# Performance work log

Measured on AMD Instinct MI355X. Metric: run time of the kernel, lower is better.

## Reference

```python
import jax, jax.numpy as jnp
import numpy as np

B, CIN, L = 4, 128, 2048
D_MODEL, D_STATE, EXPAND, HEADDIM, NGROUPS = 256, 16, 3, 3, 1
D_INNER = EXPAND * D_MODEL            # 768
NHEADS = D_INNER // HEADDIM           # 256
CONV_DIM = D_INNER + 2 * NGROUPS * D_STATE   # 800
D_IN_PROJ = 2 * D_INNER + 2 * NGROUPS * D_STATE + NHEADS  # 1824
K_PROJ, D_CONV = 4, 4
EPS = 1e-5


def setup_inputs() -> dict:
    key = jax.random.key(0)
    ks = jax.random.split(key, 9)
    x = jax.random.normal(ks[0], (B, CIN, L), jnp.float32)
    proj_w = jax.random.normal(ks[1], (D_MODEL, CIN, K_PROJ), jnp.float32) / np.float32(np.sqrt(CIN * K_PROJ))
    in_proj_w = jax.random.normal(ks[2], (D_IN_PROJ, D_MODEL), jnp.float32) / np.float32(np.sqrt(D_MODEL))
    conv_w = jax.random.normal(ks[3], (CONV_DIM, 1, D_CONV), jnp.float32) / np.float32(np.sqrt(D_CONV))
    conv_b = jax.random.normal(ks[4], (CONV_DIM,), jnp.float32) * 0.01
    # dt_bias = inverse-softplus of dt ~ LogUniform[1e-3, 1e-1] (mamba2 init)
    u = jax.random.uniform(ks[5], (NHEADS,), jnp.float32)
    dt = jnp.exp(u * np.float32(np.log(0.1) - np.log(1e-3)) + np.float32(np.log(1e-3)))
    dt_bias = dt + jnp.log(-jnp.expm1(-dt))
    A_log = jnp.log(1.0 + 15.0 * jax.random.uniform(ks[6], (NHEADS,), jnp.float32))  # A in [-16,-1]
    D_skip = jnp.ones((NHEADS,), jnp.float32)
    norm_w = jnp.ones((D_INNER,), jnp.float32)
    out_proj_w = jax.random.normal(ks[7], (D_MODEL, D_INNER), jnp.float32) / np.float32(np.sqrt(D_INNER))
    return {"x": x, "proj_w": proj_w, "in_proj_w": in_proj_w, "conv_w": conv_w,
            "conv_b": conv_b, "dt_bias": dt_bias, "A_log": A_log, "D_skip": D_skip,
            "norm_w": norm_w, "out_proj_w": out_proj_w}


def _forward(x, proj_w, in_proj_w, conv_w, conv_b, dt_bias, A_log, D_skip, norm_w, out_proj_w):
    # outer Conv1d, padding='same' (k=4 -> left 1, right 2), no bias: (B,CIN,L)->(B,D_MODEL,L)
    h = jax.lax.conv_general_dilated(x, proj_w, (1,), [(1, 2)],
                                     dimension_numbers=("NCH", "OIH", "NCH"))
    u = h.transpose(0, 2, 1)                          # (B, L, d_model)
    zxbcdt = jnp.einsum("bld,ed->ble", u, in_proj_w)  # (B, L, 1824)
    z = zxbcdt[..., :D_INNER]                                     # (B,L,768)
    xBC = zxbcdt[..., D_INNER:D_INNER + CONV_DIM]                 # (B,L,800)
    dt = zxbcdt[..., D_INNER + CONV_DIM:]                         # (B,L,256)
    dt = jax.nn.softplus(dt + dt_bias)
    # depthwise causal conv (pad d_conv-1 on left) + SiLU
    xBC_c = jax.lax.conv_general_dilated(xBC.transpose(0, 2, 1), conv_w, (1,), [(D_CONV - 1, 0)],
                                         feature_group_count=CONV_DIM,
                                         dimension_numbers=("NCH", "OIH", "NCH"))
    xBC = jax.nn.silu(xBC_c + conv_b[None, :, None]).transpose(0, 2, 1)  # (B,L,800)
    xs = xBC[..., :D_INNER].reshape(B, L, NHEADS, HEADDIM)        # (B,L,H,P)
    Bm = xBC[..., D_INNER:D_INNER + D_STATE]                      # (B,L,N) (ngroups=1)
    Cm = xBC[..., D_INNER + D_STATE:]                             # (B,L,N)
    A = -jnp.exp(A_log)                                           # (H,)

    def step(hst, inp):
        dt_t, x_t, B_t, C_t = inp                 # (B,H),(B,H,P),(B,N),(B,N)
        dA = jnp.exp(dt_t * A)[:, :, None, None]  # (B,H,1,1)
        hst = dA * hst + jnp.einsum("bh,bhp,bn->bhpn", dt_t, x_t, B_t)
        y_t = jnp.einsum("bhpn,bn->bhp", hst, C_t)
        return hst, y_t

    h0 = jnp.zeros((B, NHEADS, HEADDIM, D_STATE), x.dtype)
    _, ys = jax.lax.scan(step, h0, (dt.transpose(1, 0, 2), xs.transpose(1, 0, 2, 3),
                                    Bm.transpose(1, 0, 2), Cm.transpose(1, 0, 2)))
    y = ys.transpose(1, 0, 2, 3) + D_skip[None, None, :, None] * xs   # (B,L,H,P)
    y = y.reshape(B, L, D_INNER)
    # gated RMSNorm: gate first, then normalize (norm_before_gate=False)
    y = y * jax.nn.silu(z)
    y = y * jax.lax.rsqrt(jnp.mean(y * y, axis=-1, keepdims=True) + EPS) * norm_w
    out = jnp.einsum("ble,de->bld", y, out_proj_w)   # (B,L,d_model)
    return out.transpose(0, 2, 1)                    # (B,d_model,L)


def reference(x, proj_w, in_proj_w, conv_w, conv_b, dt_bias, A_log, D_skip, norm_w, out_proj_w):
    return _forward(x, proj_w, in_proj_w, conv_w, conv_b, dt_bias, A_log, D_skip, norm_w, out_proj_w)
```

## Files before the change

kernel.cpp:

```cpp
#include <hip/hip_runtime.h>
#include <hip/hip_fp16.h>
#include <math.h>

#define B_     4
#define CIN    128
#define LEN    2048
#define DMODEL 256
#define DSTATE 16
#define NHEADS 256
#define DINNER 768
#define CONVDIM 800
#define DINPROJ 1824
#define EPS_   1e-5f
#define CHUNK  64
#define NCHUNK 32

typedef _Float16 f16x8 __attribute__((ext_vector_type(8)));
typedef float    f32x4 __attribute__((ext_vector_type(4)));

__device__ __forceinline__ float silu_(float x){ return x / (1.0f + __expf(-x)); }
__device__ __forceinline__ float softplus_(float x){
    return x > 0.f ? x + log1pf(__expf(-x)) : log1pf(__expf(x));
}

__device__ __forceinline__ void gl2lds16(const _Float16* g, _Float16* l){
    __builtin_amdgcn_global_load_lds(
        (const __attribute__((address_space(1))) void*)g,
        (__attribute__((address_space(3))) void*)l, 16, 0, 0);
}

__global__ __launch_bounds__(256) void k_f2h3(const float* __restrict__ a0,
                                              const float* __restrict__ a1,
                                              const float* __restrict__ a2,
                                              _Float16* __restrict__ o0,
                                              _Float16* __restrict__ o1,
                                              _Float16* __restrict__ o2,
                                              int n0, int n1, int n2){
    int total = n0 + n1 + n2;
    for (int i = blockIdx.x * 256 + threadIdx.x; i < total; i += gridDim.x * 256){
        if (i < n0)            o0[i] = (_Float16)a0[i];
        else if (i < n0 + n1)  o1[i - n0] = (_Float16)a1[i - n0];
        else                   o2[i - n0 - n1] = (_Float16)a2[i - n0 - n1];
    }
}

__global__ __launch_bounds__(256) void k_im2col(const float* __restrict__ x,
                                                _Float16* __restrict__ xcol){
    __shared__ float xs[CIN][68];
    int blk = blockIdx.x;
    int b  = blk >> 5;
    int l0 = (blk & 31) << 6;
    const float* xb = x + (size_t)b * CIN * LEN;
    for (int idx = threadIdx.x; idx < CIN * 67; idx += 256){
        int ci = idx / 67, j = idx % 67;
        int gl = l0 - 1 + j;
        xs[ci][j] = (gl >= 0 && gl < LEN) ? xb[ci * LEN + gl] : 0.f;
    }
    __syncthreads();
    #pragma unroll
    for (int v = 0; v < 16; v++){
        int id = v * 256 + threadIdx.x;
        int rl = id >> 6, c = id & 63;
        f16x8 pk;
        #pragma unroll
        for (int e = 0; e < 8; e++){
            int ci = c * 2 + (e >> 2), k = e & 3;
            pk[e] = (_Float16)xs[ci][rl + k];
        }
        *(f16x8*)&xcol[((size_t)(b * LEN + l0 + rl)) * 512 + c * 8] = pk;
    }
}

template<int K, int EPI>
__global__ __launch_bounds__(256) void k_gemm(const _Float16* __restrict__ A,
                                              const _Float16* __restrict__ Bw,
                                              const float* __restrict__ dt_bias,
                                              _Float16* __restrict__ o_u,
                                              _Float16* __restrict__ o_z,
                                              _Float16* __restrict__ o_xbc,
                                              _Float16* __restrict__ o_dt,
                                              float* __restrict__ o_f){
    __shared__ __align__(16) _Float16 As[128 * 32];
    __shared__ __align__(16) _Float16 Bs[128 * 32];
    int tid  = threadIdx.x;
    int wv   = tid >> 6;
    int lane = tid & 63;
    int quad = lane >> 4;
    int l16  = lane & 15;
    int m0 = blockIdx.x * 128;
    int n0 = blockIdx.y * 128;
    int wm = (wv >> 1) * 64;
    int wn = (wv & 1) * 64;
    int srow = lane >> 2;
    int scol = (lane & 3) * 8;

    f32x4 acc[4][4];
    #pragma unroll
    for (int i = 0; i < 4; i++)
        #pragma unroll
        for (int j = 0; j < 4; j++)
            acc[i][j] = (f32x4){0.f, 0.f, 0.f, 0.f};

    for (int k0 = 0; k0 < K; k0 += 32){
        #pragma unroll
        for (int j = 0; j < 2; j++){
            int ar = m0 + wv * 32 + j * 16 + srow;
            gl2lds16(A + (size_t)ar * K + k0 + scol,
                     &As[(wv * 32 + j * 16) * 32]);
            int nr = n0 + wv * 32 + j * 16 + srow;
            if (EPI == 1) nr = nr > (DINPROJ - 1) ? (DINPROJ - 1) : nr;
            gl2lds16(Bw + (size_t)nr * K + k0 + scol,
                     &Bs[(wv * 32 + j * 16) * 32]);
        }
        __syncthreads();
        f16x8 af[4], bf[4];
        #pragma unroll
        for (int i = 0; i < 4; i++)
            af[i] = *(const f16x8*)&As[(wm + i * 16 + l16) * 32 + quad * 8];
        #pragma unroll
        for (int j = 0; j < 4; j++)
            bf[j] = *(const f16x8*)&Bs[(wn + j * 16 + l16) * 32 + quad * 8];
        #pragma unroll
        for (int i = 0; i < 4; i++)
            #pragma unroll
            for (int j = 0; j < 4; j++)
                acc[i][j] = __builtin_amdgcn_mfma_f32_16x16x32_f16(
                                af[i], bf[j], acc[i][j], 0, 0, 0);
        __syncthreads();
    }

    if (EPI == 0){
        #pragma unroll
        for (int j = 0; j < 4; j++){
            int col = n0 + wn + j * 16 + l16;
            #pragma unroll
            for (int i = 0; i < 4; i++){
                int row = m0 + wm + i * 16 + quad * 4;
                #pragma unroll
                for (int r = 0; r < 4; r++)
                    o_u[(size_t)(row + r) * DMODEL + col] = (_Float16)acc[i][j][r];
            }
        }
    } else if (EPI == 1){
        #pragma unroll
        for (int j = 0; j < 4; j++){
            int col = n0 + wn + j * 16 + l16;
            if (col < DINNER){
                #pragma unroll
                for (int i = 0; i < 4; i++){
                    int row = m0 + wm + i * 16 + quad * 4;
                    #pragma unroll
                    for (int r = 0; r < 4; r++)
                        o_z[(size_t)(row + r) * DINNER + col] = (_Float16)acc[i][j][r];
                }
            } else if (col < DINNER + CONVDIM){
                int cc = col - DINNER;
                #pragma unroll
                for (int i = 0; i < 4; i++){
                    int row = m0 + wm + i * 16 + quad * 4;
                    #pragma unroll
                    for (int r = 0; r < 4; r++)
                        o_xbc[(size_t)(row + r) * CONVDIM + cc] = (_Float16)acc[i][j][r];
                }
            } else if (col < DINPROJ){
                int hh = col - (DINNER + CONVDIM);
                float bias = dt_bias[hh];
                #pragma unroll
                for (int i = 0; i < 4; i++){
                    int row = m0 + wm + i * 16 + quad * 4;
                    #pragma unroll
                    for (int r = 0; r < 4; r++)
                        o_dt[(size_t)(row + r) * NHEADS + hh] =
                            (_Float16)softplus_(acc[i][j][r] + bias);
                }
            }
        }
    } else {
        #pragma unroll
        for (int i = 0; i < 4; i++){
            int row = m0 + wm + i * 16 + quad * 4;
            int b = row >> 11, l = row & (LEN - 1);
            #pragma unroll
            for (int j = 0; j < 4; j++){
                int d = n0 + wn + j * 16 + l16;
                *(f32x4*)&o_f[(((size_t)(b * DMODEL + d)) << 11) + l] = acc[i][j];
            }
        }
    }
}

__global__ __launch_bounds__(256) void k_dwconv(const __half* __restrict__ xbc,
                                                const float* __restrict__ cw,
                                                const float* __restrict__ cb,
                                                __half* __restrict__ xcc){
    int idx = blockIdx.x * 256 + threadIdx.x;
    int c = idx % CONVDIM;
    int r = idx / CONVDIM;
    int l = r & (LEN - 1);
    float4 wv = *(const float4*)(cw + c * 4);
    float acc = cb[c];
    if (l >= 3){
        const __half* base = xbc + (size_t)(r - 3) * CONVDIM + c;
        acc += __half2float(base[0]) * wv.x + __half2float(base[CONVDIM]) * wv.y +
               __half2float(base[2 * CONVDIM]) * wv.z + __half2float(base[3 * CONVDIM]) * wv.w;
    } else {
        const float wk[4] = {wv.x, wv.y, wv.z, wv.w};
        for (int k = 0; k < 4; k++){
            int t = l - 3 + k;
            if (t >= 0) acc += __half2float(xbc[(size_t)(r + k - 3) * CONVDIM + c]) * wk[k];
        }
    }
    xcc[idx] = __float2half(silu_(acc));
}

__global__ __launch_bounds__(64) void k_scanAC(const __half* __restrict__ dtb,
                                               const __half* __restrict__ xcc,
                                               const float* __restrict__ A_log,
                                               const float* __restrict__ D_skip,
                                               __half* __restrict__ y,
                                               __half* __restrict__ cstate,
                                               float* __restrict__ dsum){
    int blk = blockIdx.x;
    int c  = blk & (NCHUNK - 1);
    int hg = (blk >> 5) & 63;
    int b  = blk >> 11;
    int lane = threadIdx.x;
    int hl = lane >> 4;
    int n  = lane & 15;
    int h  = hg * 4 + hl;
    int c0 = h * 3;
    float A   = -__expf(A_log[h]);
    float Dsk = D_skip[h];
    int t0 = c * CHUNK;
    const __half* xr  = xcc + ((size_t)b * LEN + t0) * CONVDIM;
    const __half* dtp = dtb + ((size_t)b * LEN + t0) * NHEADS + h;
    float h0 = 0.f, h1 = 0.f, h2 = 0.f, sdt = 0.f;
    __half* yp = y + ((size_t)b * LEN + t0) * DINNER + c0;
    for (int t = 0; t < CHUNK; t++){
        float vx0 = __half2float(xr[c0]);
        float vx1 = __half2float(xr[c0 + 1]);
        float vx2 = __half2float(xr[c0 + 2]);
        float vB  = __half2float(xr[DINNER + n]);
        float vC  = __half2float(xr[DINNER + DSTATE + n]);
        float cdt = __half2float(dtp[(size_t)t * NHEADS]);
        float dA  = __expf(cdt * A);
        float dtB = cdt * vB;
        h0 = fmaf(h0, dA, vx0 * dtB);
        h1 = fmaf(h1, dA, vx1 * dtB);
        h2 = fmaf(h2, dA, vx2 * dtB);
        sdt += cdt;
        float p0 = h0 * vC, p1 = h1 * vC, p2 = h2 * vC;
        #pragma unroll
        for (int m = 1; m < 16; m <<= 1){
            p0 += __shfl_xor(p0, m, 64);
            p1 += __shfl_xor(p1, m, 64);
            p2 += __shfl_xor(p2, m, 64);
        }
        if (n < 3){
            float pv = (n == 0) ? p0 : ((n == 1) ? p1 : p2);
            float xv = (n == 0) ? vx0 : ((n == 1) ? vx1 : vx2);
            yp[n] = __float2half(fmaf(Dsk, xv, pv));
        }
        xr += CONVDIM;
        yp += DINNER;
    }
    size_t sbase = (((size_t)(b * NHEADS + h)) * NCHUNK + c) * 48;
    cstate[sbase + n]      = __float2half(h0);
    cstate[sbase + 16 + n] = __float2half(h1);
    cstate[sbase + 32 + n] = __float2half(h2);
    if (n == 0) dsum[(size_t)(b * NHEADS + h) * NCHUNK + c] = __expf(A * sdt);
}

__global__ __launch_bounds__(64) void k_scanB(__half* __restrict__ cstate,
                                              const float* __restrict__ dsum){
    int bh = blockIdx.x;
    int lane = threadIdx.x;
    if (lane >= 48) return;
    __half* st = cstate + (size_t)bh * NCHUNK * 48 + lane;
    const float* dd = dsum + (size_t)bh * NCHUNK;
    float H = 0.f;
    for (int c = 0; c < NCHUNK; c++){
        float d = dd[c];
        float s = __half2float(st[(size_t)c * 48]);
        st[(size_t)c * 48] = __float2half(H);
        H = fmaf(H, d, s);
    }
}

__global__ __launch_bounds__(256) void k_fixup(const __half* __restrict__ dtb,
                                               const __half* __restrict__ xcc,
                                               const float* __restrict__ A_log,
                                               const __half* __restrict__ cstate,
                                               __half* __restrict__ y){
    int task = blockIdx.x * 4 + (threadIdx.x >> 6);
    int lane = threadIdx.x & 63;
    int c = task & (NCHUNK - 1);
    int h = (task >> 5) & (NHEADS - 1);
    int b = task >> 13;
    float A = -__expf(A_log[h]);
    size_t row = (size_t)b * LEN + c * CHUNK + lane;
    float cum = __half2float(dtb[row * NHEADS + h]);
    #pragma unroll
    for (int m = 1; m < 64; m <<= 1){
        float v = __shfl(cum, lane - m, 64);
        if (lane >= m) cum += v;
    }
    float decay = __expf(A * cum);
    const _Float16* cp = (const _Float16*)(xcc) + row * CONVDIM + DINNER + DSTATE;
    f16x8 cv0 = *(const f16x8*)cp;
    f16x8 cv1 = *(const f16x8*)(cp + 8);
    const _Float16* hp = (const _Float16*)(cstate) + (size_t)task * 48;
    f16x8 hv[6];
    #pragma unroll
    for (int i = 0; i < 6; i++) hv[i] = *(const f16x8*)(hp + i * 8);
    float s0 = 0.f, s1 = 0.f, s2 = 0.f;
    #pragma unroll
    for (int e = 0; e < 8; e++){
        float cl = (float)cv0[e], ch = (float)cv1[e];
        s0 = fmaf(cl, (float)hv[0][e], s0); s0 = fmaf(ch, (float)hv[1][e], s0);
        s1 = fmaf(cl, (float)hv[2][e], s1); s1 = fmaf(ch, (float)hv[3][e], s1);
        s2 = fmaf(cl, (float)hv[4][e], s2); s2 = fmaf(ch, (float)hv[5][e], s2);
    }
    __half* yp = y + row * DINNER + h * 3;
    yp[0] = __float2half(__half2float(yp[0]) + decay * s0);
    yp[1] = __float2half(__half2float(yp[1]) + decay * s1);
    yp[2] = __float2half(__half2float(yp[2]) + decay * s2);
}

__global__ __launch_bounds__(256) void k_norm(__half* __restrict__ y,
                                              const __half* __restrict__ z,
                                              const float* __restrict__ nw){
    __shared__ float wsum[4];
    size_t r = blockIdx.x;
    int tid = threadIdx.x;
    const __half* zr = z + r * DINNER;
    __half* yr = y + r * DINNER;
    int e0 = tid, e1 = tid + 256, e2 = tid + 512;
    float t0 = __half2float(yr[e0]) * silu_(__half2float(zr[e0]));
    float t1 = __half2float(yr[e1]) * silu_(__half2float(zr[e1]));
    float t2 = __half2float(yr[e2]) * silu_(__half2float(zr[e2]));
    float ss = t0 * t0 + t1 * t1 + t2 * t2;
    #pragma unroll
    for (int m = 1; m < 64; m <<= 1) ss += __shfl_xor(ss, m, 64);
    if ((tid & 63) == 0) wsum[tid >> 6] = ss;
    __syncthreads();
    float tot = wsum[0] + wsum[1] + wsum[2] + wsum[3];
    float sc = rsqrtf(tot / (float)DINNER + EPS_);
    yr[e0] = __float2half(t0 * sc * nw[e0]);
    yr[e1] = __float2half(t1 * sc * nw[e1]);
    yr[e2] = __float2half(t2 * sc * nw[e2]);
}

extern "C" void kernel_launch(void* const* d_in, const int* in_sizes, int n_in,
                              void* d_out, int out_size, void* d_ws, size_t ws_size,
                              hipStream_t stream) {
    const float* x          = (const float*)d_in[0];
    const float* proj_w     = (const float*)d_in[1];
    const float* in_proj_w  = (const float*)d_in[2];
    const float* conv_w     = (const float*)d_in[3];
    const float* conv_b     = (const float*)d_in[4];
    const float* dt_bias    = (const float*)d_in[5];
    const float* A_log      = (const float*)d_in[6];
    const float* D_skip     = (const float*)d_in[7];
    const float* norm_w     = (const float*)d_in[8];
    const float* out_proj_w = (const float*)d_in[9];
    float* out = (float*)d_out;

    char* ob = (char*)d_out;
    _Float16* pw_h  = (_Float16*)ob;
    _Float16* ipw_h = (_Float16*)(ob + 262144);

    char* wsb = (char*)d_ws;
    _Float16* xcol  = (_Float16*)(wsb);
    _Float16* u_h   = (_Float16*)(wsb + 8388608);
    __half*   xcc_h = (__half*)(wsb);
    __half*   z_h   = (__half*)(wsb + 13107200);
    __half*   xbc_h = (__half*)(wsb + 25690112);
    __half*   y_h   = xbc_h;
    __half*   dt_h  = (__half*)(wsb + 38797312);
    __half*   cstate= (__half*)(wsb + 42991616);
    float*    dsum  = (float*)(wsb + 46137344);
    _Float16* opw_h = (_Float16*)(wsb + 46268416);

    k_f2h3  <<<96, 256, 0, stream>>>(proj_w, in_proj_w, out_proj_w,
                                     pw_h, ipw_h, opw_h,
                                     DMODEL * CIN * 4, DINPROJ * DMODEL,
                                     DMODEL * DINNER);
    k_im2col<<<128, 256, 0, stream>>>(x, xcol);
    k_gemm<512, 0><<<dim3(64, 2), 256, 0, stream>>>(xcol, pw_h, nullptr,
        u_h, nullptr, nullptr, nullptr, nullptr);
    k_gemm<256, 1><<<dim3(64, 15), 256, 0, stream>>>(u_h, ipw_h, dt_bias,
        nullptr, (_Float16*)z_h, (_Float16*)xbc_h, (_Float16*)dt_h, nullptr);
    k_dwconv<<<25600, 256, 0, stream>>>(xbc_h, conv_w, conv_b, xcc_h);
    k_scanAC<<<8192, 64, 0, stream>>>(dt_h, xcc_h, A_log, D_skip, y_h, cstate, dsum);
    k_scanB <<<1024, 64, 0, stream>>>(cstate, dsum);
    k_fixup <<<8192, 256, 0, stream>>>(dt_h, xcc_h, A_log, cstate, y_h);
    k_norm  <<<8192, 256, 0, stream>>>(y_h, z_h, norm_w);
    k_gemm<768, 2><<<dim3(64, 2), 256, 0, stream>>>((const _Float16*)y_h, opw_h,
        nullptr, nullptr, nullptr, nullptr, nullptr, out);
}
```

Before: 338.0 us.

## Stage scan inputs in LDS, use DPP row reductions, restructure fixup per chunk

The chunk scan now uses 256-thread blocks covering 16 heads. Each block stages the chunk's x, B/C and dt rows into shared memory with vector loads and prefetches the next timestep's values, replacing strided scalar global loads. The 16-lane shuffle reductions are replaced with DPP row-shift adds. The fixup kernel is reorganised so each block handles one half-chunk for all 256 heads: decay values are computed once into LDS and C is staged, which removes the per-task prefix-shuffle and redundant loads but cuts the grid to 256 blocks, so parallelism is much lower.

```diff
diff --git a/kernel.cpp b/kernel.cpp
--- a/kernel.cpp
+++ b/kernel.cpp
@@ -27,6 +27,15 @@
     __builtin_amdgcn_global_load_lds(
         (const __attribute__((address_space(1))) void*)g,
         (__attribute__((address_space(3))) void*)l, 16, 0, 0);
+}
+
+__device__ __forceinline__ float dpp_row_sum16(float x){
+    float v = x;
+    v += __int_as_float(__builtin_amdgcn_update_dpp(0, __float_as_int(v), 0x111, 0xf, 0xf, true));
+    v += __int_as_float(__builtin_amdgcn_update_dpp(0, __float_as_int(v), 0x112, 0xf, 0xf, true));
+    v += __int_as_float(__builtin_amdgcn_update_dpp(0, __float_as_int(v), 0x114, 0xf, 0xf, true));
+    v += __int_as_float(__builtin_amdgcn_update_dpp(0, __float_as_int(v), 0x118, 0xf, 0xf, true));
+    return v;
 }
 
 __global__ __launch_bounds__(256) void k_f2h3(const float* __restrict__ a0,
@@ -213,56 +222,87 @@
     xcc[idx] = __float2half(silu_(acc));
 }
 
-__global__ __launch_bounds__(64) void k_scanAC(const __half* __restrict__ dtb,
-                                               const __half* __restrict__ xcc,
-                                               const float* __restrict__ A_log,
-                                               const float* __restrict__ D_skip,
-                                               __half* __restrict__ y,
-                                               __half* __restrict__ cstate,
-                                               float* __restrict__ dsum){
+__global__ __launch_bounds__(256) void k_scanAC(const __half* __restrict__ dtb,
+                                                const __half* __restrict__ xcc,
+                                                const float* __restrict__ A_log,
+                                                const float* __restrict__ D_skip,
+                                                __half* __restrict__ y,
+                                                __half* __restrict__ cstate,
+                                                float* __restrict__ dsum){
+    __shared__ __align__(16) _Float16 xs_x[64][48];
+    __shared__ __align__(16) _Float16 xs_bc[64][32];
+    __shared__ __align__(16) _Float16 xs_dt[64][16];
     int blk = blockIdx.x;
-    int c  = blk & (NCHUNK - 1);
-    int hg = (blk >> 5) & 63;
-    int b  = blk >> 11;
-    int lane = threadIdx.x;
-    int hl = lane >> 4;
-    int n  = lane & 15;
-    int h  = hg * 4 + hl;
-    int c0 = h * 3;
+    int hg = blk & 15;
+    int c  = (blk >> 4) & 31;
+    int b  = blk >> 9;
+    int tid = threadIdx.x;
+    size_t row0 = (size_t)b * LEN + c * CHUNK;
+
+    const _Float16* xc16 = (const _Float16*)xcc;
+    const _Float16* dt16 = (const _Float16*)dtb;
+    #pragma unroll
+    for (int k = 0; k < 3; k++){
+        int seg = tid + k * 256;
+        if (seg < 384){
+            int t = seg / 6, k16 = seg % 6;
+            *(f16x8*)&xs_x[t][k16 * 8] =
+                *(const f16x8*)(xc16 + (row0 + t) * CONVDIM + hg * 48 + k16 * 8);
+        } else if (seg < 640){
+            int i = seg - 384; int t = i >> 2, k4 = i & 3;
+            *(f16x8*)&xs_bc[t][k4 * 8] =
+                *(const f16x8*)(xc16 + (row0 + t) * CONVDIM + DINNER + k4 * 8);
+        } else {
+            int i = seg - 640; int t = i >> 1, k2 = i & 1;
+            *(f16x8*)&xs_dt[t][k2 * 8] =
+                *(const f16x8*)(dt16 + (row0 + t) * NHEADS + hg * 16 + k2 * 8);
+        }
+    }
+    __syncthreads();
+
+    int w    = tid >> 6;
+    int lane = tid & 63;
+    int hl   = lane >> 4;
+    int n    = lane & 15;
+    int jj   = w * 4 + hl;
+    int h    = hg * 16 + jj;
+    int c0   = h * 3;
     float A   = -__expf(A_log[h]);
     float Dsk = D_skip[h];
-    int t0 = c * CHUNK;
-    const __half* xr  = xcc + ((size_t)b * LEN + t0) * CONVDIM;
-    const __half* dtp = dtb + ((size_t)b * LEN + t0) * NHEADS + h;
+
     float h0 = 0.f, h1 = 0.f, h2 = 0.f, sdt = 0.f;
-    __half* yp = y + ((size_t)b * LEN + t0) * DINNER + c0;
+    __half* yp = y + row0 * DINNER + c0;
+    float vx0 = (float)xs_x[0][jj * 3 + 0];
+    float vx1 = (float)xs_x[0][jj * 3 + 1];
+    float vx2 = (float)xs_x[0][jj * 3 + 2];
+    float vB  = (float)xs_bc[0][n];
+    float vC  = (float)xs_bc[0][16 + n];
+    float cdt = (float)xs_dt[0][jj];
     for (int t = 0; t < CHUNK; t++){
-        float vx0 = __half2float(xr[c0]);
-        float vx1 = __half2float(xr[c0 + 1]);
-        float vx2 = __half2float(xr[c0 + 2]);
-        float vB  = __half2float(xr[DINNER + n]);
-        float vC  = __half2float(xr[DINNER + DSTATE + n]);
-        float cdt = __half2float(dtp[(size_t)t * NHEADS]);
+        int tn = (t + 1 < CHUNK) ? t + 1 : t;
+        float nx0 = (float)xs_x[tn][jj * 3 + 0];
+        float nx1 = (float)xs_x[tn][jj * 3 + 1];
+        float nx2 = (float)xs_x[tn][jj * 3 + 2];
+        float nB  = (float)xs_bc[tn][n];
+        float nC  = (float)xs_bc[tn][16 + n];
+        float ndt = (float)xs_dt[tn][jj];
+
         float dA  = __expf(cdt * A);
         float dtB = cdt * vB;
         h0 = fmaf(h0, dA, vx0 * dtB);
         h1 = fmaf(h1, dA, vx1 * dtB);
         h2 = fmaf(h2, dA, vx2 * dtB);
         sdt += cdt;
-        float p0 = h0 * vC, p1 = h1 * vC, p2 = h2 * vC;
-        #pragma unroll
-        for (int m = 1; m < 16; m <<= 1){
-            p0 += __shfl_xor(p0, m, 64);
-            p1 += __shfl_xor(p1, m, 64);
-            p2 += __shfl_xor(p2, m, 64);
-        }
-        if (n < 3){
-            float pv = (n == 0) ? p0 : ((n == 1) ? p1 : p2);
-            float xv = (n == 0) ? vx0 : ((n == 1) ? vx1 : vx2);
-            yp[n] = __float2half(fmaf(Dsk, xv, pv));
-        }
-        xr += CONVDIM;
+        float p0 = dpp_row_sum16(h0 * vC);
+        float p1 = dpp_row_sum16(h1 * vC);
+        float p2 = dpp_row_sum16(h2 * vC);
+        if (n == 15){
+            yp[0] = __float2half(fmaf(Dsk, vx0, p0));
+            yp[1] = __float2half(fmaf(Dsk, vx1, p1));
+            yp[2] = __float2half(fmaf(Dsk, vx2, p2));
+        }
         yp += DINNER;
+        vx0 = nx0; vx1 = nx1; vx2 = nx2; vB = nB; vC = nC; cdt = ndt;
     }
     size_t sbase = (((size_t)(b * NHEADS + h)) * NCHUNK + c) * 48;
     cstate[sbase + n]      = __float2half(h0);
@@ -292,39 +332,60 @@
                                                const float* __restrict__ A_log,
                                                const __half* __restrict__ cstate,
                                                __half* __restrict__ y){
-    int task = blockIdx.x * 4 + (threadIdx.x >> 6);
-    int lane = threadIdx.x & 63;
-    int c = task & (NCHUNK - 1);
-    int h = (task >> 5) & (NHEADS - 1);
-    int b = task >> 13;
-    float A = -__expf(A_log[h]);
-    size_t row = (size_t)b * LEN + c * CHUNK + lane;
-    float cum = __half2float(dtb[row * NHEADS + h]);
+    __shared__ __align__(16) _Float16 decay[32][256];
+    __shared__ __align__(16) _Float16 Cs[32][16];
+    int blk = blockIdx.x;
+    int th = blk & 1;
+    int c  = (blk >> 1) & 31;
+    int b  = blk >> 6;
+    int tid = threadIdx.x;
+    int base_t = th * 32;
+    size_t row0 = (size_t)b * LEN + c * CHUNK;
+
+    if (tid < 64){
+        int i = tid >> 1, k = tid & 1;
+        *(f16x8*)&Cs[i][k * 8] =
+            *(const f16x8*)((const _Float16*)xcc +
+                            (row0 + base_t + i) * CONVDIM + DINNER + DSTATE + k * 8);
+    }
+    {
+        float A = -__expf(A_log[tid]);
+        float cum = 0.f;
+        const _Float16* dp = (const _Float16*)dtb + row0 * NHEADS + tid;
+        for (int t = 0; t < CHUNK; t++){
+            cum += (float)dp[(size_t)t * NHEADS];
+            if (t >= base_t && t < base_t + 32)
+                decay[t - base_t][tid] = (_Float16)__expf(A * cum);
+        }
+    }
+    __syncthreads();
+
+    const _Float16* hp = (const _Float16*)cstate +
+                         (((size_t)(b * NHEADS + tid)) * NCHUNK + c) * 48;
+    float Hi[3][16];
     #pragma unroll
-    for (int m = 1; m < 64; m <<= 1){
-        float v = __shfl(cum, lane - m, 64);
-        if (lane >= m) cum += v;
-    }
-    float decay = __expf(A * cum);
-    const _Float16* cp = (const _Float16*)(xcc) + row * CONVDIM + DINNER + DSTATE;
-    f16x8 cv0 = *(const f16x8*)cp;
-    f16x8 cv1 = *(const f16x8*)(cp + 8);
-    const _Float16* hp = (const _Float16*)(cstate) + (size_t)task * 48;
-    f16x8 hv[6];
-    #pragma unroll
-    for (int i = 0; i < 6; i++) hv[i] = *(const f16x8*)(hp + i * 8);
-    float s0 = 0.f, s1 = 0.f, s2 = 0.f;
-    #pragma unroll
-    for (int e = 0; e < 8; e++){
-        float cl = (float)cv0[e], ch = (float)cv1[e];
-        s0 = fmaf(cl, (float)hv[0][e], s0); s0 = fmaf(ch, (float)hv[1][e], s0);
-        s1 = fmaf(cl, (float)hv[2][e], s1); s1 = fmaf(ch, (float)hv[3][e], s1);
-        s2 = fmaf(cl, (float)hv[4][e], s2); s2 = fmaf(ch, (float)hv[5][e], s2);
-    }
-    __half* yp = y + row * DINNER + h * 3;
-    yp[0] = __float2half(__half2float(yp[0]) + decay * s0);
-    yp[1] = __float2half(__half2float(yp[1]) + decay * s1);
-    yp[2] = __float2half(__half2float(yp[2]) + decay * s2);
+    for (int p = 0; p < 3; p++){
+        f16x8 a = *(const f16x8*)(hp + p * 16);
+        f16x8 bq = *(const f16x8*)(hp + p * 16 + 8);
+        #pragma unroll
+        for (int e = 0; e < 8; e++){ Hi[p][e] = (float)a[e]; Hi[p][8 + e] = (float)bq[e]; }
+    }
+    __half* yb = y + (row0 + base_t) * DINNER + tid * 3;
+    for (int i = 0; i < 32; i++){
+        float s0 = 0.f, s1 = 0.f, s2 = 0.f;
+        #pragma unroll
+        for (int nn = 0; nn < 16; nn++){
+            float cv = (float)Cs[i][nn];
+            s0 = fmaf(cv, Hi[0][nn], s0);
+            s1 = fmaf(cv, Hi[1][nn], s1);
+            s2 = fmaf(cv, Hi[2][nn], s2);
+        }
+        float d = (float)decay[i][tid];
+        __half* yp = yb + (size_t)i * DINNER;
+        yp[0] = __float2half(__half2float(yp[0]) + d * s0);
+        yp[1] = __float2half(__half2float(yp[1]) + d * s1);
+        yp[2] = __float2half(__half2float(yp[2]) + d * s2);
+    }
 }
 
 __global__ __launch_bounds__(256) void k_norm(__half* __restrict__ y,
@@ -392,9 +453,9 @@
     k_gemm<256, 1><<<dim3(64, 15), 256, 0, stream>>>(u_h, ipw_h, dt_bias,
         nullptr, (_Float16*)z_h, (_Float16*)xbc_h, (_Float16*)dt_h, nullptr);
     k_dwconv<<<25600, 256, 0, stream>>>(xbc_h, conv_w, conv_b, xcc_h);
-    k_scanAC<<<8192, 64, 0, stream>>>(dt_h, xcc_h, A_log, D_skip, y_h, cstate, dsum);
+    k_scanAC<<<2048, 256, 0, stream>>>(dt_h, xcc_h, A_log, D_skip, y_h, cstate, dsum);
     k_scanB <<<1024, 64, 0, stream>>>(cstate, dsum);
-    k_fixup <<<8192, 256, 0, stream>>>(dt_h, xcc_h, A_log, cstate, y_h);
+    k_fixup <<<256, 256, 0, stream>>>(dt_h, xcc_h, A_log, cstate, y_h);
     k_norm  <<<8192, 256, 0, stream>>>(y_h, z_h, norm_w);
     k_gemm<768, 2><<<dim3(64, 2), 256, 0, stream>>>((const _Float16*)y_h, opw_h,
         nullptr, nullptr, nullptr, nullptr, nullptr, out);
```

Result: slower. 367.2 us (+8.6%).

## Vectorize depthwise conv, pack scan waves into blocks, restructure fixup per chunk

Applied to the files above, without the earlier changes.

The depthwise conv now has each thread handle 8 channels with 16-byte half vector loads and stores, replacing scalar per-channel accesses. The chunk scan packs four wave tasks into each 256-thread block instead of launching one 64-thread block per task. The fixup kernel is reorganised so each block covers one (batch, chunk, half-chunk) and each thread one head. Per-step decays and C vectors are staged in shared memory and the carried state is kept in registers, replacing a per-lane shuffle prefix sum and repeated state loads. The trade-off is that only 256 fixup blocks are launched, each running a serial 64-step cumulative sum, and the per-head y updates write 6-byte strided pieces.

```diff
diff --git a/kernel.cpp b/kernel.cpp
--- a/kernel.cpp
+++ b/kernel.cpp
@@ -194,37 +194,41 @@
                                                 const float* __restrict__ cb,
                                                 __half* __restrict__ xcc){
     int idx = blockIdx.x * 256 + threadIdx.x;
-    int c = idx % CONVDIM;
-    int r = idx / CONVDIM;
-    int l = r & (LEN - 1);
-    float4 wv = *(const float4*)(cw + c * 4);
-    float acc = cb[c];
-    if (l >= 3){
-        const __half* base = xbc + (size_t)(r - 3) * CONVDIM + c;
-        acc += __half2float(base[0]) * wv.x + __half2float(base[CONVDIM]) * wv.y +
-               __half2float(base[2 * CONVDIM]) * wv.z + __half2float(base[3 * CONVDIM]) * wv.w;
-    } else {
-        const float wk[4] = {wv.x, wv.y, wv.z, wv.w};
-        for (int k = 0; k < 4; k++){
-            int t = l - 3 + k;
-            if (t >= 0) acc += __half2float(xbc[(size_t)(r + k - 3) * CONVDIM + c]) * wk[k];
-        }
-    }
-    xcc[idx] = __float2half(silu_(acc));
-}
-
-__global__ __launch_bounds__(64) void k_scanAC(const __half* __restrict__ dtb,
-                                               const __half* __restrict__ xcc,
-                                               const float* __restrict__ A_log,
-                                               const float* __restrict__ D_skip,
-                                               __half* __restrict__ y,
-                                               __half* __restrict__ cstate,
-                                               float* __restrict__ dsum){
-    int blk = blockIdx.x;
-    int c  = blk & (NCHUNK - 1);
-    int hg = (blk >> 5) & 63;
-    int b  = blk >> 11;
-    int lane = threadIdx.x;
+    int seg = idx % 100;
+    int r   = idx / 100;
+    int l   = r & (LEN - 1);
+    int c8  = seg * 8;
+    const _Float16* base = (const _Float16*)xbc + (size_t)r * CONVDIM + c8;
+    f16x8 zv = {0, 0, 0, 0, 0, 0, 0, 0};
+    f16x8 x3 = *(const f16x8*)base;
+    f16x8 x2 = (l >= 1) ? *(const f16x8*)(base - CONVDIM) : zv;
+    f16x8 x1 = (l >= 2) ? *(const f16x8*)(base - 2 * CONVDIM) : zv;
+    f16x8 x0 = (l >= 3) ? *(const f16x8*)(base - 3 * CONVDIM) : zv;
+    f16x8 o;
+    #pragma unroll
+    for (int e = 0; e < 8; e++){
+        float4 wv = *(const float4*)(cw + (size_t)(c8 + e) * 4);
+        float acc = cb[c8 + e]
+                  + (float)x0[e] * wv.x + (float)x1[e] * wv.y
+                  + (float)x2[e] * wv.z + (float)x3[e] * wv.w;
+        o[e] = (_Float16)silu_(acc);
+    }
+    *(f16x8*)((_Float16*)xcc + (size_t)r * CONVDIM + c8) = o;
+}
+
+__global__ __launch_bounds__(256) void k_scanAC(const __half* __restrict__ dtb,
+                                                const __half* __restrict__ xcc,
+                                                const float* __restrict__ A_log,
+                                                const float* __restrict__ D_skip,
+                                                __half* __restrict__ y,
+                                                __half* __restrict__ cstate,
+                                                float* __restrict__ dsum){
+    int wave = threadIdx.x >> 6;
+    int task = blockIdx.x * 4 + wave;
+    int c  = task & (NCHUNK - 1);
+    int hg = (task >> 5) & 63;
+    int b  = task >> 11;
+    int lane = threadIdx.x & 63;
     int hl = lane >> 4;
     int n  = lane & 15;
     int h  = hg * 4 + hl;
@@ -292,39 +296,60 @@
                                                const float* __restrict__ A_log,
                                                const __half* __restrict__ cstate,
                                                __half* __restrict__ y){
-    int task = blockIdx.x * 4 + (threadIdx.x >> 6);
-    int lane = threadIdx.x & 63;
-    int c = task & (NCHUNK - 1);
-    int h = (task >> 5) & (NHEADS - 1);
-    int b = task >> 13;
-    float A = -__expf(A_log[h]);
-    size_t row = (size_t)b * LEN + c * CHUNK + lane;
-    float cum = __half2float(dtb[row * NHEADS + h]);
+    __shared__ __align__(16) _Float16 decay[32][256];
+    __shared__ __align__(16) _Float16 Cs[32][16];
+    int blk = blockIdx.x;
+    int th = blk & 1;
+    int c  = (blk >> 1) & 31;
+    int b  = blk >> 6;
+    int tid = threadIdx.x;
+    int base_t = th * 32;
+    size_t row0 = (size_t)b * LEN + c * CHUNK;
+
+    if (tid < 64){
+        int i = tid >> 1, k = tid & 1;
+        *(f16x8*)&Cs[i][k * 8] =
+            *(const f16x8*)((const _Float16*)xcc +
+                            (row0 + base_t + i) * CONVDIM + DINNER + DSTATE + k * 8);
+    }
+    {
+        float A = -__expf(A_log[tid]);
+        float cum = 0.f;
+        const _Float16* dp = (const _Float16*)dtb + row0 * NHEADS + tid;
+        for (int t = 0; t < CHUNK; t++){
+            cum += (float)dp[(size_t)t * NHEADS];
+            if (t >= base_t && t < base_t + 32)
+                decay[t - base_t][tid] = (_Float16)__expf(A * cum);
+        }
+    }
+    __syncthreads();
+
+    const _Float16* hp = (const _Float16*)cstate +
+                         (((size_t)(b * NHEADS + tid)) * NCHUNK + c) * 48;
+    float Hi[3][16];
     #pragma unroll
-    for (int m = 1; m < 64; m <<= 1){
-        float v = __shfl(cum, lane - m, 64);
-        if (lane >= m) cum += v;
-    }
-    float decay = __expf(A * cum);
-    const _Float16* cp = (const _Float16*)(xcc) + row * CONVDIM + DINNER + DSTATE;
-    f16x8 cv0 = *(const f16x8*)cp;
-    f16x8 cv1 = *(const f16x8*)(cp + 8);
-    const _Float16* hp = (const _Float16*)(cstate) + (size_t)task * 48;
-    f16x8 hv[6];
-    #pragma unroll
-    for (int i = 0; i < 6; i++) hv[i] = *(const f16x8*)(hp + i * 8);
-    float s0 = 0.f, s1 = 0.f, s2 = 0.f;
-    #pragma unroll
-    for (int e = 0; e < 8; e++){
-        float cl = (float)cv0[e], ch = (float)cv1[e];
-        s0 = fmaf(cl, (float)hv[0][e], s0); s0 = fmaf(ch, (float)hv[1][e], s0);
-        s1 = fmaf(cl, (float)hv[2][e], s1); s1 = fmaf(ch, (float)hv[3][e], s1);
-        s2 = fmaf(cl, (float)hv[4][e], s2); s2 = fmaf(ch, (float)hv[5][e], s2);
-    }
-    __half* yp = y + row * DINNER + h * 3;
-    yp[0] = __float2half(__half2float(yp[0]) + decay * s0);
-    yp[1] = __float2half(__half2float(yp[1]) + decay * s1);
-    yp[2] = __float2half(__half2float(yp[2]) + decay * s2);
+    for (int p = 0; p < 3; p++){
+        f16x8 a = *(const f16x8*)(hp + p * 16);
+        f16x8 bq = *(const f16x8*)(hp + p * 16 + 8);
+        #pragma unroll
+        for (int e = 0; e < 8; e++){ Hi[p][e] = (float)a[e]; Hi[p][8 + e] = (float)bq[e]; }
+    }
+    __half* yb = y + (row0 + base_t) * DINNER + tid * 3;
+    for (int i = 0; i < 32; i++){
+        float s0 = 0.f, s1 = 0.f, s2 = 0.f;
+        #pragma unroll
+        for (int nn = 0; nn < 16; nn++){
+            float cv = (float)Cs[i][nn];
+            s0 = fmaf(cv, Hi[0][nn], s0);
+            s1 = fmaf(cv, Hi[1][nn], s1);
+            s2 = fmaf(cv, Hi[2][nn], s2);
+        }
+        float d = (float)decay[i][tid];
+        __half* yp = yb + (size_t)i * DINNER;
+        yp[0] = __float2half(__half2float(yp[0]) + d * s0);
+        yp[1] = __float2half(__half2float(yp[1]) + d * s1);
+        yp[2] = __float2half(__half2float(yp[2]) + d * s2);
+    }
 }
 
 __global__ __launch_bounds__(256) void k_norm(__half* __restrict__ y,
@@ -391,10 +416,10 @@
         u_h, nullptr, nullptr, nullptr, nullptr);
     k_gemm<256, 1><<<dim3(64, 15), 256, 0, stream>>>(u_h, ipw_h, dt_bias,
         nullptr, (_Float16*)z_h, (_Float16*)xbc_h, (_Float16*)dt_h, nullptr);
-    k_dwconv<<<25600, 256, 0, stream>>>(xbc_h, conv_w, conv_b, xcc_h);
-    k_scanAC<<<8192, 64, 0, stream>>>(dt_h, xcc_h, A_log, D_skip, y_h, cstate, dsum);
+    k_dwconv<<<3200, 256, 0, stream>>>(xbc_h, conv_w, conv_b, xcc_h);
+    k_scanAC<<<2048, 256, 0, stream>>>(dt_h, xcc_h, A_log, D_skip, y_h, cstate, dsum);
     k_scanB <<<1024, 64, 0, stream>>>(cstate, dsum);
-    k_fixup <<<8192, 256, 0, stream>>>(dt_h, xcc_h, A_log, cstate, y_h);
+    k_fixup <<<256, 256, 0, stream>>>(dt_h, xcc_h, A_log, cstate, y_h);
     k_norm  <<<8192, 256, 0, stream>>>(y_h, z_h, norm_w);
     k_gemm<768, 2><<<dim3(64, 2), 256, 0, stream>>>((const _Float16*)y_h, opw_h,
         nullptr, nullptr, nullptr, nullptr, nullptr, out);
```

Result: faster. 320.3 us (-5.2%).
